# Kernel tuning notes

Hardware: AMD Instinct MI355X
Metric: run time of the kernel (lower is better)

## Reference

```python
import jax, jax.numpy as jnp
import numpy as np

N_NODES = 100000


def setup_inputs() -> dict:
    key = jax.random.key(0)
    ks = jax.random.split(key, 7)
    n, d, c, e = N_NODES, 256, 128, 3200000
    features = jax.random.normal(ks[0], (n, d), dtype=jnp.float32)
    adj_row = jax.random.randint(ks[1], (e,), 0, n, dtype=jnp.int32)
    adj_col = jax.random.randint(ks[2], (e,), 0, n, dtype=jnp.int32)
    adj_vals = jax.random.uniform(ks[3], (e,), dtype=jnp.float32)
    kernel = jax.random.normal(ks[4], (d, c), dtype=jnp.float32) * (1.0 / np.sqrt(d))
    bias = jax.random.normal(ks[5], (c,), dtype=jnp.float32) * 0.01
    skip_weight = jax.random.normal(ks[6], (c,), dtype=jnp.float32)
    return {"features": features, "adj_row": adj_row, "adj_col": adj_col,
            "adj_vals": adj_vals, "kernel": kernel, "bias": bias,
            "skip_weight": skip_weight}


def reference(features, adj_row, adj_col, adj_vals, kernel, bias, skip_weight):
    # h = X @ W  : [n, c]
    h = features @ kernel
    # SpMM: out[r] += A[r, c] * h[c] over edges (COO)
    msgs = adj_vals[:, None] * h[adj_col]            # [e, c]
    agg = jax.ops.segment_sum(msgs, adj_row, num_segments=N_NODES)  # [n, c]
    out = h * skip_weight + agg                      # skip-connection scale + aggregation
    out = out + bias
    return jax.nn.selu(out)
```

## Files before the change

kernel.cpp:

```cpp
#include <hip/hip_runtime.h>
#include <math.h>

#define N_NODES 100000
#define D 256
#define C 128
#define N_EDGES 3200000

#define BROWS 128
#define NBUCKET ((N_NODES + BROWS - 1) / BROWS)
#define CAP 4608
#define EPB 8192
#define PBLOCKS ((N_EDGES + EPB - 1) / EPB)
#define NCH 13
#define NKEY (BROWS * NCH)

#define GROWS 128
#define NGB ((N_NODES + GROWS - 1) / GROWS)
#define KH 128
#define XPAD 136

typedef __attribute__((ext_vector_type(8))) short bf16x8;
typedef __attribute__((ext_vector_type(4))) float f32x4;

__device__ __forceinline__ unsigned short f2bf(float f) {
  const unsigned int u = __float_as_uint(f);
  return (unsigned short)((u + 0x7fffu + ((u >> 16) & 1u)) >> 16);
}
__device__ __forceinline__ unsigned int pack_bf(float lo, float hi) {
  return (unsigned int)f2bf(lo) | ((unsigned int)f2bf(hi) << 16);
}
__device__ __forceinline__ float bflo(unsigned int u) {
  return __uint_as_float(u << 16);
}
__device__ __forceinline__ float bfhi(unsigned int u) {
  return __uint_as_float(u & 0xffff0000u);
}
__device__ __forceinline__ float selu1(float x) {
  const float scale = 1.0507009873554804934193349852946f;
  const float alpha = 1.6732632423543772848170429916717f;
  return x > 0.f ? scale * x : scale * alpha * (__expf(x) - 1.f);
}
__device__ __forceinline__ unsigned int pack_rec(int col, float val) {
  return ((unsigned int)col << 15) | ((unsigned int)f2bf(val) & 0x7fffu);
}
__device__ __forceinline__ float rec_val(unsigned int r) {
  return __uint_as_float((r & 0x7fffu) << 16);
}

__global__ __launch_bounds__(256) void prep(const float* __restrict__ W,
                                            unsigned short* __restrict__ WT) {
  const int t = blockIdx.x * blockDim.x + threadIdx.x;
  const int n = t >> 8;
  const int k = t & 255;
  WT[t] = f2bf(W[k * C + n]);
}

__global__ __launch_bounds__(512) void gemm_partition(
    const float* __restrict__ X, const unsigned short* __restrict__ WT,
    unsigned short* __restrict__ h2, const int* __restrict__ row,
    const int* __restrict__ col, const float* __restrict__ vals,
    unsigned int* __restrict__ meta, uint2* __restrict__ recs) {
  __shared__ unsigned short xs[GROWS][XPAD];
  __shared__ int hist[NBUCKET];
  __shared__ int scanA[1024];
  __shared__ int scanB[1024];
  const int bid = blockIdx.x;
  const int tid = threadIdx.x;
  const int rem = bid % 3;

  if (rem != 2) {
    const int gid = (bid / 3) * 2 + rem;
    const int rows0 = gid * GROWS;
    const int lane = tid & 63;
    const int w = tid >> 6;
    const int r = lane & 15;
    const int kg = lane >> 4;

    f32x4 acc[8];
#pragma unroll
    for (int f = 0; f < 8; ++f) acc[f] = (f32x4){0.f, 0.f, 0.f, 0.f};

#pragma unroll
    for (int h = 0; h < 2; ++h) {
#pragma unroll
      for (int i = 0; i < 8; ++i) {
        const int lrow = w * 16 + i * 2 + (lane >> 5);
        const int grow = rows0 + lrow;
        const int kc = (lane & 31) * 4;
        f32x4 x = (f32x4){0.f, 0.f, 0.f, 0.f};
        if (grow < N_NODES)
          x = *reinterpret_cast<const f32x4*>(X + (size_t)grow * D + h * KH +
                                              kc);
        const unsigned int p0 = pack_bf(x[0], x[1]);
        const unsigned int p1 = pack_bf(x[2], x[3]);
        *reinterpret_cast<uint2*>(&xs[lrow][kc]) = make_uint2(p0, p1);
      }
      __syncthreads();
#pragma unroll
      for (int ks = 0; ks < 4; ++ks) {
        const bf16x8 a =
            *reinterpret_cast<const bf16x8*>(&xs[w * 16 + r][ks * 32 + kg * 8]);
#pragma unroll
        for (int f = 0; f < 8; ++f) {
          const bf16x8 bf = *reinterpret_cast<const bf16x8*>(
              WT + (size_t)(f * 16 + r) * D + h * KH + ks * 32 + kg * 8);
          acc[f] =
              __builtin_amdgcn_mfma_f32_16x16x32_bf16(a, bf, acc[f], 0, 0, 0);
        }
      }
      __syncthreads();
    }
#pragma unroll
    for (int f = 0; f < 8; ++f)
#pragma unroll
      for (int j = 0; j < 4; ++j) {
        const int grow = rows0 + w * 16 + kg * 4 + j;
        if (grow < N_NODES) h2[(size_t)grow * C + f * 16 + r] = f2bf(acc[f][j]);
      }
  } else {
    const int pb = bid / 3;
    const int e0 = pb * EPB;
    for (int i = tid; i < NBUCKET; i += 512) hist[i] = 0;
    __syncthreads();

    unsigned int stash[16];
#pragma unroll
    for (int k = 0; k < 16; ++k) {
      const int e = e0 + k * 512 + tid;
      unsigned int s = 0xFFFFFFFFu;
      if (e < N_EDGES) {
        const int r = __builtin_nontemporal_load(row + e);
        const int off = atomicAdd(&hist[r >> 7], 1);
        s = (unsigned int)r | ((unsigned int)off << 17);
      }
      stash[k] = s;
    }
    __syncthreads();

    for (int i = tid; i < 1024; i += 512) scanA[i] = (i < NBUCKET) ? hist[i] : 0;
    __syncthreads();
    int* src = scanA;
    int* dst = scanB;
    for (int off = 1; off < 1024; off <<= 1) {
      for (int i = tid; i < 1024; i += 512)
        dst[i] = src[i] + ((i >= off) ? src[i - off] : 0);
      __syncthreads();
      int* tp = src;
      src = dst;
      dst = tp;
    }
    for (int b = tid; b < NBUCKET; b += 512) {
      const int sb = src[b] - hist[b];
      dst[b] = sb;
      meta[(size_t)pb * NBUCKET + b] =
          ((unsigned int)sb << 16) | (unsigned int)hist[b];
    }
    __syncthreads();

#pragma unroll
    for (int k = 0; k < 16; ++k) {
      const unsigned int s = stash[k];
      if (s == 0xFFFFFFFFu) continue;
      const int r = (int)(s & 0x1FFFFu);
      const int off = (int)(s >> 17);
      const int e = e0 + k * 512 + tid;
      const int c = __builtin_nontemporal_load(col + e);
      const float v = __builtin_nontemporal_load(vals + e);
      const int b = r >> 7;
      recs[(size_t)pb * EPB + dst[b] + off] =
          make_uint2(pack_rec(c, v), r & (BROWS - 1));
    }
  }
}

__global__ __launch_bounds__(512) void sort_gather_selu(
    const unsigned int* __restrict__ meta, const uint2* __restrict__ recs,
    const unsigned int* __restrict__ h2u, const float* __restrict__ skip,
    const float* __restrict__ bias, float* __restrict__ out) {
  __shared__ unsigned int sorted[CAP];
  __shared__ int hist[NKEY];
  __shared__ int start[2048];
  __shared__ int segA[512];
  __shared__ int segB[512];
  __shared__ unsigned int segglob[PBLOCKS];
  const int tid = threadIdx.x;
  const int b = blockIdx.x;

  int cnt = 0;
  if (tid < PBLOCKS) {
    const unsigned int m = meta[(size_t)tid * NBUCKET + b];
    cnt = (int)(m & 0xFFFFu);
    segglob[tid] = (unsigned int)tid * EPB + (m >> 16);
  }
  segA[tid] = cnt;
  for (int i = tid; i < NKEY; i += 512) hist[i] = 0;
  __syncthreads();
  int* s1 = segA;
  int* s2 = segB;
  for (int off = 1; off < 512; off <<= 1) {
    s2[tid] = s1[tid] + ((tid >= off) ? s1[tid - off] : 0);
    __syncthreads();
    int* tp = s1;
    s1 = s2;
    s2 = tp;
  }
  const int fill0 = s1[PBLOCKS - 1];
  const int fill = fill0 < CAP ? fill0 : CAP;

  uint2 stash[9];
  int nst = 0;
  for (int i = tid; i < fill; i += 512) {
    int lo = 0, hi = PBLOCKS - 1;
    while (lo < hi) {
      const int mid = (lo + hi) >> 1;
      if (s1[mid] > i) hi = mid;
      else lo = mid + 1;
    }
    const int idx = i - (lo ? s1[lo - 1] : 0);
    const unsigned long long rc = __builtin_nontemporal_load(
        reinterpret_cast<const unsigned long long*>(recs) + segglob[lo] + idx);
    const unsigned int cv = (unsigned int)rc;
    const unsigned int lr = (unsigned int)(rc >> 32);
    const unsigned int key = lr * NCH + (cv >> 28);
    const int off = atomicAdd(&hist[key], 1);
    stash[nst] = make_uint2(cv, key | ((unsigned int)off << 11));
    ++nst;
  }
  __syncthreads();

  for (int i = tid; i < 2048; i += 512) start[i] = (i < NKEY) ? hist[i] : 0;
  __syncthreads();
  for (int off = 1; off < 2048; off <<= 1) {
    int t[4];
#pragma unroll
    for (int q = 0; q < 4; ++q) {
      const int idx = tid + q * 512;
      t[q] = (idx >= off) ? start[idx - off] : 0;
    }
    __syncthreads();
#pragma unroll
    for (int q = 0; q < 4; ++q) start[tid + q * 512] += t[q];
    __syncthreads();
  }

  for (int k = 0; k < nst; ++k) {
    const int key = (int)(stash[k].y & 2047u);
    const int off = (int)(stash[k].y >> 11);
    sorted[start[key] - hist[key] + off] = stash[k].x;
  }
  __syncthreads();

  const int lane = tid & 63;
  const int wv = tid >> 6;
  for (int lr = wv; lr < BROWS; lr += 8) {
    const int grow = b * BROWS + lr;
    if (grow >= N_NODES) break;
    const int k0 = lr * NCH;
    const int je = start[k0 + NCH - 1];
    int j = start[k0] - hist[k0];
    float ax = 0.f, ay = 0.f;
    for (; j + 7 < je; j += 8) {
      unsigned int cc[8], uu[8];
#pragma unroll
      for (int q = 0; q < 8; ++q) cc[q] = sorted[j + q];
#pragma unroll
      for (int q = 0; q < 8; ++q) uu[q] = h2u[(size_t)(cc[q] >> 15) * 64 + lane];
#pragma unroll
      for (int q = 0; q < 8; ++q) {
        ax = fmaf(rec_val(cc[q]), bflo(uu[q]), ax);
        ay = fmaf(rec_val(cc[q]), bfhi(uu[q]), ay);
      }
    }
    for (; j + 3 < je; j += 4) {
      unsigned int cc[4], uu[4];
#pragma unroll
      for (int q = 0; q < 4; ++q) cc[q] = sorted[j + q];
#pragma unroll
      for (int q = 0; q < 4; ++q) uu[q] = h2u[(size_t)(cc[q] >> 15) * 64 + lane];
#pragma unroll
      for (int q = 0; q < 4; ++q) {
        ax = fmaf(rec_val(cc[q]), bflo(uu[q]), ax);
        ay = fmaf(rec_val(cc[q]), bfhi(uu[q]), ay);
      }
    }
    for (; j < je; ++j) {
      const unsigned int cc = sorted[j];
      const unsigned int u = h2u[(size_t)(cc >> 15) * 64 + lane];
      ax = fmaf(rec_val(cc), bflo(u), ax);
      ay = fmaf(rec_val(cc), bfhi(u), ay);
    }
    const unsigned int hr = h2u[(size_t)grow * 64 + lane];
    const float2 sk = *reinterpret_cast<const float2*>(skip + lane * 2);
    const float2 bi = *reinterpret_cast<const float2*>(bias + lane * 2);
    const float ox = selu1(fmaf(bflo(hr), sk.x, ax) + bi.x);
    const float oy = selu1(fmaf(bfhi(hr), sk.y, ay) + bi.y);
    *reinterpret_cast<float2*>(out + (size_t)grow * C + lane * 2) =
        make_float2(ox, oy);
  }
}

extern "C" void kernel_launch(void* const* d_in, const int* in_sizes, int n_in,
                              void* d_out, int out_size, void* d_ws,
                              size_t ws_size, hipStream_t stream) {
  const float* features = (const float*)d_in[0];
  const int* adj_row = (const int*)d_in[1];
  const int* adj_col = (const int*)d_in[2];
  const float* adj_vals = (const float*)d_in[3];
  const float* W = (const float*)d_in[4];
  const float* bias = (const float*)d_in[5];
  const float* skip = (const float*)d_in[6];
  float* out = (float*)d_out;

  char* ws = (char*)d_ws;
  const size_t SZ_H2 = (size_t)N_NODES * C * 2;
  const size_t OFF_RECS = (SZ_H2 + 255) & ~(size_t)255;
  const size_t SZ_RECS = (size_t)PBLOCKS * EPB * 8;
  const size_t OFF_META = OFF_RECS + SZ_RECS;
  const size_t SZ_META = (size_t)PBLOCKS * NBUCKET * 4;
  const size_t OFF_WT = (OFF_META + SZ_META + 255) & ~(size_t)255;
  const size_t NEEDED = OFF_WT + (size_t)D * C * 2;

  if (ws_size < NEEDED) return;

  unsigned short* h2 = (unsigned short*)ws;
  uint2* recs = (uint2*)(ws + OFF_RECS);
  unsigned int* meta = (unsigned int*)(ws + OFF_META);
  unsigned short* WT = (unsigned short*)(ws + OFF_WT);

  prep<<<(D * C) / 256, 256, 0, stream>>>(W, WT);

  gemm_partition<<<3 * PBLOCKS, 512, 0, stream>>>(
      features, WT, h2, adj_row, adj_col, adj_vals, meta, recs);

  sort_gather_selu<<<NBUCKET, 512, 0, stream>>>(
      meta, recs, (const unsigned int*)h2, skip, bias, out);
}
```

Baseline: 267.8 us.

## Replace chunked-key counting sort with two-pass per-row bucketing over segments

The sort_gather_selu kernel no longer sorts by (row, column-chunk) keys with a global prefix scan, binary search and register stash. Instead each wave walks whole segments, builds a per-row histogram, scans only 128 entries, then rereads the records to scatter them into shared memory. This removes the large 2048-entry scan and the binary search. In exchange the records are read twice from global memory, and the column-chunk ordering that may have improved locality in h2 gathers is lost. An unused packA_nt helper is also added.

```diff
diff --git a/kernel.cpp b/kernel.cpp
--- a/kernel.cpp
+++ b/kernel.cpp
@@ -11,8 +11,6 @@
 #define CAP 4608
 #define EPB 8192
 #define PBLOCKS ((N_EDGES + EPB - 1) / EPB)
-#define NCH 13
-#define NKEY (BROWS * NCH)
 
 #define GROWS 128
 #define NGB ((N_NODES + GROWS - 1) / GROWS)
@@ -45,6 +43,20 @@
 }
 __device__ __forceinline__ float rec_val(unsigned int r) {
   return __uint_as_float((r & 0x7fffu) << 16);
+}
+__device__ __forceinline__ bf16x8 packA_nt(const float* p) {
+  const f32x4 a0 = __builtin_nontemporal_load(reinterpret_cast<const f32x4*>(p));
+  const f32x4 a1 =
+      __builtin_nontemporal_load(reinterpret_cast<const f32x4*>(p) + 1);
+  union {
+    unsigned int u[4];
+    bf16x8 v;
+  } af;
+  af.u[0] = pack_bf(a0[0], a0[1]);
+  af.u[1] = pack_bf(a0[2], a0[3]);
+  af.u[2] = pack_bf(a1[0], a1[1]);
+  af.u[3] = pack_bf(a1[2], a1[3]);
+  return af.v;
 }
 
 __global__ __launch_bounds__(256) void prep(const float* __restrict__ W,
@@ -178,86 +190,73 @@
     const unsigned int* __restrict__ h2u, const float* __restrict__ skip,
     const float* __restrict__ bias, float* __restrict__ out) {
   __shared__ unsigned int sorted[CAP];
-  __shared__ int hist[NKEY];
-  __shared__ int start[2048];
-  __shared__ int segA[512];
-  __shared__ int segB[512];
-  __shared__ unsigned int segglob[PBLOCKS];
+  __shared__ int hist[BROWS];
+  __shared__ int start[BROWS];
+  __shared__ int cur[BROWS];
+  __shared__ int segcnt[512];
+  __shared__ unsigned int segglob[512];
   const int tid = threadIdx.x;
   const int b = blockIdx.x;
-
-  int cnt = 0;
+  const int lane = tid & 63;
+  const int wv = tid >> 6;
+
   if (tid < PBLOCKS) {
     const unsigned int m = meta[(size_t)tid * NBUCKET + b];
-    cnt = (int)(m & 0xFFFFu);
+    segcnt[tid] = (int)(m & 0xFFFFu);
     segglob[tid] = (unsigned int)tid * EPB + (m >> 16);
-  }
-  segA[tid] = cnt;
-  for (int i = tid; i < NKEY; i += 512) hist[i] = 0;
+  } else {
+    segcnt[tid] = 0;
+    segglob[tid] = 0;
+  }
+  if (tid < BROWS) {
+    hist[tid] = 0;
+    cur[tid] = 0;
+  }
   __syncthreads();
-  int* s1 = segA;
-  int* s2 = segB;
-  for (int off = 1; off < 512; off <<= 1) {
-    s2[tid] = s1[tid] + ((tid >= off) ? s1[tid - off] : 0);
-    __syncthreads();
-    int* tp = s1;
-    s1 = s2;
-    s2 = tp;
-  }
-  const int fill0 = s1[PBLOCKS - 1];
-  const int fill = fill0 < CAP ? fill0 : CAP;
-
-  uint2 stash[9];
-  int nst = 0;
-  for (int i = tid; i < fill; i += 512) {
-    int lo = 0, hi = PBLOCKS - 1;
-    while (lo < hi) {
-      const int mid = (lo + hi) >> 1;
-      if (s1[mid] > i) hi = mid;
-      else lo = mid + 1;
-    }
-    const int idx = i - (lo ? s1[lo - 1] : 0);
-    const unsigned long long rc = __builtin_nontemporal_load(
-        reinterpret_cast<const unsigned long long*>(recs) + segglob[lo] + idx);
-    const unsigned int cv = (unsigned int)rc;
-    const unsigned int lr = (unsigned int)(rc >> 32);
-    const unsigned int key = lr * NCH + (cv >> 28);
-    const int off = atomicAdd(&hist[key], 1);
-    stash[nst] = make_uint2(cv, key | ((unsigned int)off << 11));
-    ++nst;
+
+  const unsigned long long* recs64 =
+      reinterpret_cast<const unsigned long long*>(recs);
+
+  for (int seg = wv; seg < PBLOCKS; seg += 8) {
+    const int cnt = segcnt[seg];
+    const unsigned int base = segglob[seg];
+    for (int i = lane; i < cnt; i += 64) {
+      const unsigned long long rc = recs64[base + i];
+      atomicAdd(&hist[(int)(rc >> 32)], 1);
+    }
   }
   __syncthreads();
 
-  for (int i = tid; i < 2048; i += 512) start[i] = (i < NKEY) ? hist[i] : 0;
+  if (tid < BROWS) start[tid] = hist[tid];
   __syncthreads();
-  for (int off = 1; off < 2048; off <<= 1) {
-    int t[4];
-#pragma unroll
-    for (int q = 0; q < 4; ++q) {
-      const int idx = tid + q * 512;
-      t[q] = (idx >= off) ? start[idx - off] : 0;
-    }
-    __syncthreads();
-#pragma unroll
-    for (int q = 0; q < 4; ++q) start[tid + q * 512] += t[q];
-    __syncthreads();
-  }
-
-  for (int k = 0; k < nst; ++k) {
-    const int key = (int)(stash[k].y & 2047u);
-    const int off = (int)(stash[k].y >> 11);
-    sorted[start[key] - hist[key] + off] = stash[k].x;
+  for (int off = 1; off < BROWS; off <<= 1) {
+    int t = 0;
+    if (tid < BROWS && tid >= off) t = start[tid - off];
+    __syncthreads();
+    if (tid < BROWS) start[tid] += t;
+    __syncthreads();
+  }
+
+  for (int seg = wv; seg < PBLOCKS; seg += 8) {
+    const int cnt = segcnt[seg];
+    const unsigned int base = segglob[seg];
+    for (int i = lane; i < cnt; i += 64) {
+      const unsigned long long rc = recs64[base + i];
+      const int lr = (int)(rc >> 32);
+      const int off = atomicAdd(&cur[lr], 1);
+      const int pos = start[lr] - hist[lr] + off;
+      if (pos < CAP) sorted[pos] = (unsigned int)rc;
+    }
   }
   __syncthreads();
 
-  const int lane = tid & 63;
-  const int wv = tid >> 6;
   for (int lr = wv; lr < BROWS; lr += 8) {
     const int grow = b * BROWS + lr;
     if (grow >= N_NODES) break;
-    const int k0 = lr * NCH;
-    const int je = start[k0 + NCH - 1];
-    int j = start[k0] - hist[k0];
+    int j = start[lr] - hist[lr];
+    int je = start[lr];
+    if (je > CAP) je = CAP;
+    if (j > je) j = je;
     float ax = 0.f, ay = 0.f;
     for (; j + 7 < je; j += 8) {
       unsigned int cc[8], uu[8];
```

Result: slower. 287.7 us (+7.4%).
